# Kernel tuning notes

Hardware: AMD Instinct MI355X
Metric: run time of the kernel (lower is better)

Reference implementation:

```python
import jax, jax.numpy as jnp
import numpy as np

IN_CH, OUT_CH, K, UP = 512, 256, 3, 2
WSCALE = float(1.0 / np.sqrt(K * K * IN_CH))  # use_wscale gain / sqrt(fan_in), lr_mul=1
ACT_GAIN = float(np.sqrt(2.0))                # lrelu def_gain
CLAMP = 256.0                                  # conv_clamp * runtime_gain(=1)
FIR_PAD = 1                                    # px0+pxt = px1+pxt = 1 (derived in forward)

def _fir_filter():
    # upfirdn2d.setup_filter([1,3,3,1]): outer product then normalize to sum 1
    f1 = jnp.array([1.0, 3.0, 3.0, 1.0], jnp.float32)
    f2 = jnp.outer(f1, f1)
    return f2 / jnp.sum(f2)  # (4,4), sums to 1

def setup_inputs() -> dict:
    key = jax.random.key(0)
    k1, k2 = jax.random.split(key)
    return {
        "x": jax.random.normal(k1, (16, IN_CH, 64, 64), jnp.float32),
        "weight": jax.random.normal(k2, (OUT_CH, IN_CH, K, K), jnp.float32),
        "bias": jnp.zeros((OUT_CH,), jnp.float32),
    }

def _forward(x, weight, bias):
    w = weight * WSCALE  # runtime weight scaling
    # torch conv_transpose2d(x, w.transpose(0,1), stride=UP, padding=0)
    # == lhs-dilated correlation with spatially flipped kernel, pad K-1 each side
    k = w[:, :, ::-1, ::-1]
    y = jax.lax.conv_general_dilated(
        x, k, window_strides=(1, 1),
        padding=((K - 1, K - 1), (K - 1, K - 1)),
        lhs_dilation=(UP, UP),
        dimension_numbers=('NCHW', 'OIHW', 'NCHW'))  # (N, OUT_CH, 129, 129)
    # upfirdn2d(up=1, padding=(1,1,1,1), gain=UP**2):
    # pad, then depthwise conv with flipped filter scaled by gain**(ndim/2)=UP*UP
    f = _fir_filter() * (UP * UP)
    y = jnp.pad(y, ((0, 0), (0, 0), (FIR_PAD, FIR_PAD), (FIR_PAD, FIR_PAD)))
    fk = jnp.broadcast_to(f[::-1, ::-1][None, None], (OUT_CH, 1, 4, 4))
    y = jax.lax.conv_general_dilated(
        y, fk, (1, 1), 'VALID',
        feature_group_count=OUT_CH,
        dimension_numbers=('NCHW', 'OIHW', 'NCHW'))  # (N, OUT_CH, 128, 128)
    # bias_act: bias add, leaky_relu(0.2), gain sqrt(2), clamp +-256
    y = y + bias[None, :, None, None]
    y = jnp.where(y >= 0, y, 0.2 * y) * ACT_GAIN
    return jnp.clip(y, -CLAMP, CLAMP)

def reference(x, weight, bias):
    return _forward(x, weight, bias)
```

## Files before the change

kernel.cpp:

```cpp
#include <hip/hip_runtime.h>
#include <hip/hip_bf16.h>

#define NIMG 16
#define IN_CH 512
#define OUT_CH 256
#define HIN 64
#define HOUT 128
#define HP 66

#define WSCALE 0.014731391f
#define ACT_GAIN 1.41421356237f
#define CLAMP_V 256.0f

typedef __attribute__((ext_vector_type(8))) short bf16x8;
typedef __attribute__((ext_vector_type(4))) float f32x4;
typedef __attribute__((ext_vector_type(16))) float f32x16;

__device__ __constant__ float c_G[2][3][3] = {
    {{0.00f, 0.25f, 0.75f}, {0.75f, 0.75f, 0.25f}, {0.25f, 0.00f, 0.00f}},
    {{0.00f, 0.00f, 0.25f}, {0.25f, 0.75f, 0.75f}, {0.75f, 0.25f, 0.00f}}
};

#define XBF_BYTES ((size_t)NIMG * 64 * HP * HP * 16)
#define EBF_BYTES ((size_t)9 * 64 * 1024 * 16)
#define WS_NEED (XBF_BYTES + EBF_BYTES)

__global__ __launch_bounds__(256) void xpose_kernel(const float* __restrict__ x,
                                                    __hip_bfloat16* __restrict__ xbf) {
    const int n = blockIdx.z;
    const int hp = blockIdx.y;
    const int c0 = blockIdx.x << 6;
    const int tid = threadIdx.x;
    const int sgb = c0 >> 3;
    const bf16x8 zero = {0, 0, 0, 0, 0, 0, 0, 0};

    if (hp == 0 || hp == HP - 1) {
        for (int idx = tid; idx < 8 * HP; idx += 256) {
            int s3 = idx / HP, wp = idx - s3 * HP;
            size_t a = (((size_t)(n * 64 + sgb + s3) * HP + hp) * HP + wp);
            *(bf16x8*)((char*)xbf + a * 16) = zero;
        }
        return;
    }
    __shared__ float tile[64][65];
    {
        int cc = tid >> 6, w = tid & 63;
        for (int cb = 0; cb < 64; cb += 4)
            tile[cb + cc][w] =
                x[(((size_t)n * IN_CH + c0 + cb + cc) * HIN + (hp - 1)) * HIN + w];
    }
    __syncthreads();
    {
        int s3 = tid >> 5, wq = tid & 31;
#pragma unroll
        for (int wb = 0; wb < 64; wb += 32) {
            int wimg = wb + wq;
            bf16x8 v;
#pragma unroll
            for (int k = 0; k < 8; ++k) {
                __hip_bfloat16 b = __float2bfloat16(tile[s3 * 8 + k][wimg]);
                v[k] = *reinterpret_cast<short*>(&b);
            }
            size_t a = (((size_t)(n * 64 + sgb + s3) * HP + hp) * HP + (wimg + 1));
            *(bf16x8*)((char*)xbf + a * 16) = v;
        }
        if (tid < 16) {
            int s3h = tid >> 1, wph = (tid & 1) ? (HP - 1) : 0;
            size_t a = (((size_t)(n * 64 + sgb + s3h) * HP + hp) * HP + wph);
            *(bf16x8*)((char*)xbf + a * 16) = zero;
        }
    }
}

__global__ __launch_bounds__(256) void build_ebf_kernel(const float* __restrict__ w,
                                                        __hip_bfloat16* __restrict__ ebf) {
    int gid = blockIdx.x * 256 + threadIdx.x;
    if (gid >= OUT_CH * IN_CH) return;
    int oc = gid >> 9, c = gid & 511;
    int sg = c >> 3, ce = c & 7;
    float wm[3][3];
    const float* wp = w + (size_t)gid * 9;
#pragma unroll
    for (int a = 0; a < 3; ++a)
#pragma unroll
        for (int b = 0; b < 3; ++b) wm[a][b] = wp[a * 3 + b] * WSCALE;
#pragma unroll
    for (int i = 0; i < 3; ++i)
#pragma unroll
        for (int j = 0; j < 3; ++j)
#pragma unroll
            for (int pu = 0; pu < 2; ++pu)
#pragma unroll
                for (int pv = 0; pv < 2; ++pv) {
                    float s = 0.f;
#pragma unroll
                    for (int a = 0; a < 3; ++a)
#pragma unroll
                        for (int b = 0; b < 3; ++b)
                            s += wm[a][b] * c_G[pu][i][a] * c_G[pv][j][b];
                    int row = oc * 4 + pu * 2 + pv;
                    ebf[(((size_t)(i * 3 + j) * 64 + sg) * 1024 + row) * 8 + ce] =
                        __float2bfloat16(s);
                }
}

#define MFMA4(AF, BF)                                                                       \
    do {                                                                                    \
        acc[0] = __builtin_amdgcn_mfma_f32_32x32x16_bf16((AF)[0], (BF)[0], acc[0], 0, 0, 0);\
        acc[1] = __builtin_amdgcn_mfma_f32_32x32x16_bf16((AF)[0], (BF)[1], acc[1], 0, 0, 0);\
        acc[2] = __builtin_amdgcn_mfma_f32_32x32x16_bf16((AF)[1], (BF)[0], acc[2], 0, 0, 0);\
        acc[3] = __builtin_amdgcn_mfma_f32_32x32x16_bf16((AF)[1], (BF)[1], acc[3], 0, 0, 0);\
    } while (0)

#define ASTEP 557568
#define AJ_FJ (-3902960)
#define AJ_FI (-3901952)
#define BSTEP 131072
#define DAK1(PAR) (((((PAR) ^ 1) << 2) | 1) << 14)
#define DBK1(PAR) (((((PAR) ^ 1) << 2) | 3) << 14)
#define DAK0(PAR) ((((PAR) << 2) | 0) << 14)
#define DBK0(PAR) ((((PAR) << 2) | 2) << 14)

#define GLL(SRC, DSTOFF)                                                          \
    __builtin_amdgcn_global_load_lds(                                             \
        (const __attribute__((address_space(1))) unsigned int*)(SRC),             \
        (__attribute__((address_space(3))) unsigned int*)(ldsW + (DSTOFF)), 16, 0, 0)

#define TILE_ITER(PAR, TT, SP01, SP23, VMS, LGK3, LAST)                           \
    {                                                                             \
        const int PB = (PAR) ? 65536 : 0;                                         \
                     \
        aO[0] = *(const bf16x8*)&lds[A0 + PB + 8192];                             \
        aO[1] = *(const bf16x8*)&lds[A1 + PB + 8192];                             \
        bO[0] = *(const bf16x8*)&lds[B0 + PB + 8192];                             \
        bO[1] = *(const bf16x8*)&lds[B1 + PB + 8192];                             \
        if (SP01) GLL(xbc + sA1 + voffA, DAK1(PAR));                              \
        sA1 += (((TT) & 7) == 6) ? (((TT) == 22 || (TT) == 46) ? AJ_FI : AJ_FJ)   \
                                 : ASTEP;                                         \
        asm volatile("s_waitcnt lgkmcnt(4)" ::: "memory");                        \
        __builtin_amdgcn_sched_barrier(0);                                        \
        __builtin_amdgcn_s_setprio(1);                                            \
        MFMA4(aE, bE);                                                            \
        __builtin_amdgcn_s_setprio(0);                                            \
        asm volatile("s_waitcnt " VMS ::: "memory");                              \
        __builtin_amdgcn_s_barrier();                                             \
        __builtin_amdgcn_sched_barrier(0);                                        \
                     \
        aE[0] = *(const bf16x8*)&lds[A0 + PB + 16384];                            \
        aE[1] = *(const bf16x8*)&lds[A1 + PB + 16384];                            \
        bE[0] = *(const bf16x8*)&lds[B0 + PB + 16384];                            \
        bE[1] = *(const bf16x8*)&lds[B1 + PB + 16384];                            \
        if (SP01) GLL(ebc + sB1 + voffB, DBK1(PAR));                              \
        sB1 += BSTEP;                                                             \
        asm volatile("s_waitcnt lgkmcnt(4)" ::: "memory");                        \
        __builtin_amdgcn_sched_barrier(0);                                        \
        __builtin_amdgcn_s_setprio(1);                                            \
        MFMA4(aO, bO);                                                            \
        __builtin_amdgcn_s_setprio(0);                                            \
        __builtin_amdgcn_s_barrier();                                             \
        __builtin_amdgcn_sched_barrier(0);                                        \
                     \
        aO[0] = *(const bf16x8*)&lds[A0 + PB + 24576];                            \
        aO[1] = *(const bf16x8*)&lds[A1 + PB + 24576];                            \
        bO[0] = *(const bf16x8*)&lds[B0 + PB + 24576];                            \
        bO[1] = *(const bf16x8*)&lds[B1 + PB + 24576];                            \
        if (SP23) GLL(xbc + sA0 + voffA, DAK0(PAR));                              \
        sA0 += (((TT) & 7) == 5) ? (((TT) == 21 || (TT) == 45) ? AJ_FI : AJ_FJ)   \
                                 : ASTEP;                                         \
        asm volatile("s_waitcnt lgkmcnt(4)" ::: "memory");                        \
        __builtin_amdgcn_sched_barrier(0);                                        \
        __builtin_amdgcn_s_setprio(1);                                            \
        MFMA4(aE, bE);                                                            \
        __builtin_amdgcn_s_setprio(0);                                            \
        asm volatile("s_waitcnt " VMS ::: "memory");                              \
        __builtin_amdgcn_s_barrier();                                             \
        __builtin_amdgcn_sched_barrier(0);                                        \
           \
        if (!(LAST)) {                                                            \
            const int NB = (PAR) ? 0 : 65536;                                     \
            aE[0] = *(const bf16x8*)&lds[A0 + NB];                                \
            aE[1] = *(const bf16x8*)&lds[A1 + NB];                                \
            bE[0] = *(const bf16x8*)&lds[B0 + NB];                                \
            bE[1] = *(const bf16x8*)&lds[B1 + NB];                                \
        }                                                                         \
        if (SP23) GLL(ebc + sB0 + voffB, DBK0(PAR));                              \
        sB0 += BSTEP;                                                             \
        asm volatile("s_waitcnt " LGK3 ::: "memory");                             \
        __builtin_amdgcn_sched_barrier(0);                                        \
        __builtin_amdgcn_s_setprio(1);                                            \
        MFMA4(aO, bO);                                                            \
        __builtin_amdgcn_s_setprio(0);                                            \
        __builtin_amdgcn_s_barrier();                                             \
        __builtin_amdgcn_sched_barrier(0);                                        \
    }

__global__ __launch_bounds__(1024) void mfma_conv8_kernel(
    const __hip_bfloat16* __restrict__ xbf, const __hip_bfloat16* __restrict__ ebf,
    const float* __restrict__ bias, float* __restrict__ out) {
    __shared__ __align__(16) char lds[131072];

    const int tid = threadIdx.x;
    const int lane = tid & 63;
    const int wid = tid >> 6;
    const int wy = wid >> 2;
    const int wx = wid & 3;

    const int bid = blockIdx.x;
    const int wkid = ((bid & 7) << 7) + (bid >> 3);
    const int mtile = wkid >> 2;
    const int ntile = wkid & 3;
    const int n = mtile >> 4;
    const int sub = mtile & 15;
    const int qh0 = (sub >> 2) << 4;
    const int qw0 = (sub & 3) << 4;
    const int n0 = ntile << 8;

    const int slice = wid & 3;
    const int rb = wid >> 2;

    f32x16 acc[4];
#pragma unroll
    for (int j = 0; j < 4; ++j) acc[j] = (f32x16)(0.f);

    char* ldsW = lds + (slice << 12) + (rb << 10);
    const char* xbc = (const char*)xbf;
    const char* ebc = (const char*)ebf;

    const int q = lane ^ ((lane & 32) ? 4 : 0) ^ ((slice & 1) ? 4 : 0);
    const int voffA =
        ((((n << 6) + slice) * HP + qh0 + (rb << 2) + (q >> 4)) * HP + qw0 +
         (q & 15)) * 16;
    const int voffB = (slice << 14) + ((n0 + (rb << 6) + q) << 4);

    auto stage = [&](int s) {
        const int tt2 = s >> 2;
        const int part = s & 3;
        const int mat = part & 1;
        const int kh = part >> 1;
        const int slot = (((tt2 & 1) << 2) | (mat << 1) | kh) << 14;
        const int sg = (tt2 << 3) + (kh << 2);
        const char* src = mat == 0 ? (xbc + voffA + sg * 69696)
                                   : (ebc + voffB + sg * 16384);
        GLL(src, slot);
    };

    const int sl = lane >> 5;
    const int l31 = lane & 31;
    const int sx = sl ? 64 : 0;
    const int A0 = (sl << 12) + (wy << 10) + ((l31 << 4) ^ sx);
    const int A1 = (sl << 12) + (wy << 10) + 512 + ((l31 << 4) ^ 64 ^ sx);
    const int B0 = 32768 + (sl << 12) + (wx << 10) + ((l31 << 4) ^ sx);
    const int B1 = 32768 + (sl << 12) + (wx << 10) + 512 + ((l31 << 4) ^ 64 ^ sx);

    int sA1 = 12 * 69696;
    int sA0 = 16 * 69696;
    int sB1 = 12 * 16384;
    int sB0 = 16 * 16384;

#pragma unroll
    for (int s = 0; s < 6; ++s) stage(s);
    asm volatile("s_waitcnt vmcnt(2)" ::: "memory");
    __builtin_amdgcn_s_barrier();
    __builtin_amdgcn_sched_barrier(0);

    bf16x8 aE[2], aO[2], bE[2], bO[2];
    aE[0] = *(const bf16x8*)&lds[A0];
    aE[1] = *(const bf16x8*)&lds[A1];
    bE[0] = *(const bf16x8*)&lds[B0];
    bE[1] = *(const bf16x8*)&lds[B1];

#pragma unroll 1
    for (int tt = 0; tt < 68; tt += 2) {
        TILE_ITER(0, tt, 1, 1, "vmcnt(3)", "lgkmcnt(4)", 0);
        TILE_ITER(1, tt + 1, 1, 1, "vmcnt(3)", "lgkmcnt(4)", 0);
    }
    TILE_ITER(0, 68, 1, 1, "vmcnt(3)", "lgkmcnt(4)", 0);
    TILE_ITER(1, 69, 1, 1, "vmcnt(0)", "lgkmcnt(4)", 0);
    TILE_ITER(0, 70, 1, 0, "vmcnt(0)", "lgkmcnt(4)", 0);
    TILE_ITER(1, 71, 0, 0, "vmcnt(0)", "lgkmcnt(0)", 1);

    float bv[2];
#pragma unroll
    for (int nt = 0; nt < 2; ++nt)
        bv[nt] = bias[(n0 + (wx << 6) + (nt << 5) + l31) >> 2];
#pragma unroll
    for (int j = 0; j < 4; ++j) {
        const int mt = j >> 1, nt = j & 1;
        const int nn = n0 + (wx << 6) + (nt << 5) + l31;
        const int oc = nn >> 2, pu = (nn >> 1) & 1, pv = nn & 1;
#pragma unroll
        for (int v = 0; v < 16; ++v) {
            const int m = (wy << 6) + (mt << 5) + (v & 3) + ((v >> 2) << 3) + (sl << 2);
            const int qr = m >> 4, qc = m & 15;
            const int hb = 2 * (qh0 + qr), wb = 2 * (qw0 + qc);
            float val = acc[j][v] + bv[nt];
            val = (val >= 0.f ? val : 0.2f * val) * ACT_GAIN;
            val = fminf(fmaxf(val, -CLAMP_V), CLAMP_V);
            out[(((size_t)n * OUT_CH + oc) * HOUT + (hb + pu)) * HOUT + (wb + pv)] = val;
        }
    }
}

__global__ void build_e_kernel(const float* __restrict__ w, float* __restrict__ e_ws) {
    int gid = blockIdx.x * blockDim.x + threadIdx.x;
    if (gid >= OUT_CH * IN_CH) return;
    float wm[3][3];
    const float* wp = w + (size_t)gid * 9;
#pragma unroll
    for (int a = 0; a < 3; ++a)
#pragma unroll
        for (int b = 0; b < 3; ++b) wm[a][b] = wp[a * 3 + b] * WSCALE;
    float* op = e_ws + (size_t)gid * 36;
#pragma unroll
    for (int i = 0; i < 3; ++i)
#pragma unroll
        for (int j = 0; j < 3; ++j)
#pragma unroll
            for (int pu = 0; pu < 2; ++pu)
#pragma unroll
                for (int pv = 0; pv < 2; ++pv) {
                    float s = 0.f;
#pragma unroll
                    for (int a = 0; a < 3; ++a)
#pragma unroll
                        for (int b = 0; b < 3; ++b)
                            s += wm[a][b] * c_G[pu][i][a] * c_G[pv][j][b];
                    op[(i * 3 + j) * 4 + pu * 2 + pv] = s;
                }
}

#define OGB 8
#define CB 8
#define QT 16
__global__ __launch_bounds__(256) void fused_conv_kernel(
    const float* __restrict__ x, const float* __restrict__ e_ws,
    const float* __restrict__ bias, float* __restrict__ out) {
    __shared__ float sX[CB][18][19];
    __shared__ float4 sE[OGB * CB * 9];
    const int tid = threadIdx.x;
    const int o2 = tid >> 7;
    const int qy = (tid >> 3) & 15;
    const int qxp = tid & 7;
    const int tileIdx = blockIdx.x;
    const int hq0 = (tileIdx >> 2) * QT;
    const int wq0 = (tileIdx & 3) * QT;
    const int o0 = blockIdx.y * OGB;
    const int n = blockIdx.z;
    float4 acc[2][4];
#pragma unroll
    for (int q = 0; q < 2; ++q)
#pragma unroll
        for (int oo = 0; oo < 4; ++oo) acc[q][oo] = make_float4(0.f, 0.f, 0.f, 0.f);
    for (int c0 = 0; c0 < IN_CH; c0 += CB) {
        for (int idx = tid; idx < CB * 18 * 18; idx += 256) {
            int cc = idx / 324;
            int rem = idx - cc * 324;
            int r = rem / 18;
            int col = rem - r * 18;
            int h = hq0 - 1 + r;
            int ww = wq0 - 1 + col;
            float v = 0.f;
            if (h >= 0 && h < HIN && ww >= 0 && ww < HIN)
                v = x[(((size_t)n * IN_CH + (c0 + cc)) * HIN + h) * HIN + ww];
            sX[cc][r][col] = v;
        }
        {
            float* sEf = (float*)sE;
            for (int idx = tid; idx < OGB * CB * 36; idx += 256) {
                int ol = idx / (CB * 36);
                int rem = idx - ol * (CB * 36);
                sEf[ol * (CB * 36) + rem] =
                    e_ws[((size_t)(o0 + ol) * IN_CH + c0) * 36 + rem];
            }
        }
        __syncthreads();
#pragma unroll 1
        for (int cc = 0; cc < CB; ++cc) {
#pragma unroll
            for (int i = 0; i < 3; ++i) {
#pragma unroll
                for (int j = 0; j < 3; ++j) {
                    float xv0 = sX[cc][qy + i][2 * qxp + j];
                    float xv1 = sX[cc][qy + i][2 * qxp + 1 + j];
#pragma unroll
                    for (int oo = 0; oo < 4; ++oo) {
                        float4 e = sE[((o2 * 4 + oo) * CB + cc) * 9 + i * 3 + j];
                        acc[0][oo].x += xv0 * e.x; acc[0][oo].y += xv0 * e.y;
                        acc[0][oo].z += xv0 * e.z; acc[0][oo].w += xv0 * e.w;
                        acc[1][oo].x += xv1 * e.x; acc[1][oo].y += xv1 * e.y;
                        acc[1][oo].z += xv1 * e.z; acc[1][oo].w += xv1 * e.w;
                    }
                }
            }
        }
        __syncthreads();
    }
#pragma unroll
    for (int q = 0; q < 2; ++q) {
        int qx = 2 * qxp + q;
        int u0 = 2 * (hq0 + qy);
        int v0 = 2 * (wq0 + qx);
#pragma unroll
        for (int oo = 0; oo < 4; ++oo) {
            int o = o0 + o2 * 4 + oo;
            float b = bias[o];
            float vals[4] = {acc[q][oo].x, acc[q][oo].y, acc[q][oo].z, acc[q][oo].w};
#pragma unroll
            for (int p = 0; p < 4; ++p) {
                int pu = p >> 1, pv = p & 1;
                float v = vals[p] + b;
                v = (v >= 0.f ? v : 0.2f * v) * ACT_GAIN;
                v = fminf(fmaxf(v, -CLAMP_V), CLAMP_V);
                out[(((size_t)n * OUT_CH + o) * HOUT + (u0 + pu)) * HOUT + (v0 + pv)] = v;
            }
        }
    }
}

extern "C" void kernel_launch(void* const* d_in, const int* in_sizes, int n_in,
                              void* d_out, int out_size, void* d_ws, size_t ws_size,
                              hipStream_t stream) {
    const float* x = (const float*)d_in[0];
    const float* w = (const float*)d_in[1];
    const float* bias = (const float*)d_in[2];
    float* out = (float*)d_out;

    if (ws_size >= WS_NEED) {
        __hip_bfloat16* xbf = (__hip_bfloat16*)d_ws;
        __hip_bfloat16* ebf = (__hip_bfloat16*)((char*)d_ws + XBF_BYTES);
        xpose_kernel<<<dim3(8, HP, NIMG), 256, 0, stream>>>(x, xbf);
        build_ebf_kernel<<<(OUT_CH * IN_CH + 255) / 256, 256, 0, stream>>>(w, ebf);
        mfma_conv8_kernel<<<dim3(1024), 1024, 0, stream>>>(xbf, ebf, bias, out);
    } else {
        float* e_ws = (float*)d_ws;
        build_e_kernel<<<(OUT_CH * IN_CH + 255) / 256, 256, 0, stream>>>(w, e_ws);
        dim3 grid(16, OUT_CH / OGB, NIMG);
        fused_conv_kernel<<<grid, 256, 0, stream>>>(x, e_ws, bias, out);
    }
}
```

Before: 651.3 us.

## Replace fine-grained staggered LDS prefetch with simple whole-tile double buffering

Replaces the staggered per-quarter prefetch pipeline, which issued one global-to-LDS load per sub-step and placed a barrier after every MFMA group, with a simpler scheme. Each tile now issues all four loads for the next buffer at its start, runs four MFMA groups, then waits on vmcnt(0) and does one barrier per tile. This cuts barrier count and simplifies waitcnt bookkeeping. In exchange the prefetch distance shrinks to one tile and every tile ends with a full memory drain, so load latency may be exposed.

```diff
diff --git a/kernel.cpp b/kernel.cpp
--- a/kernel.cpp
+++ b/kernel.cpp
@@ -116,82 +116,73 @@
 #define AJ_FJ (-3902960)
 #define AJ_FI (-3901952)
 #define BSTEP 131072
-#define DAK1(PAR) (((((PAR) ^ 1) << 2) | 1) << 14)
-#define DBK1(PAR) (((((PAR) ^ 1) << 2) | 3) << 14)
-#define DAK0(PAR) ((((PAR) << 2) | 0) << 14)
-#define DBK0(PAR) ((((PAR) << 2) | 2) << 14)
 
 #define GLL(SRC, DSTOFF)                                                          \
     __builtin_amdgcn_global_load_lds(                                             \
         (const __attribute__((address_space(1))) unsigned int*)(SRC),             \
         (__attribute__((address_space(3))) unsigned int*)(ldsW + (DSTOFF)), 16, 0, 0)
 
-#define TILE_ITER(PAR, TT, SP01, SP23, VMS, LGK3, LAST)                           \
+#define TILE_ITER(PAR, TT, SP, LAST)                                              \
     {                                                                             \
-        const int PB = (PAR) ? 65536 : 0;                                         \
-                     \
+        const int PB = (PAR) << 16;                                               \
+        const int NPB = ((PAR) ^ 1) << 16;                                        \
+            \
+        if (SP) {                                                                 \
+            GLL(xbc + sA0 + voffA, NPB);                                          \
+            GLL(xbc + sA1 + voffA, NPB + 16384);                                  \
+            GLL(ebc + sB0 + voffB, NPB + 32768);                                  \
+            GLL(ebc + sB1 + voffB, NPB + 49152);                                  \
+        }                                                                         \
+        sA0 += (((TT) & 7) == 6) ? (((TT) == 22 || (TT) == 46) ? AJ_FI : AJ_FJ)   \
+                                 : ASTEP;                                         \
+        sA1 += (((TT) & 7) == 6) ? (((TT) == 22 || (TT) == 46) ? AJ_FI : AJ_FJ)   \
+                                 : ASTEP;                                         \
+        sB0 += BSTEP;                                                             \
+        sB1 += BSTEP;                                                             \
+                                                  \
+        aE[0] = *(const bf16x8*)&lds[A0 + PB];                                    \
+        aE[1] = *(const bf16x8*)&lds[A1 + PB];                                    \
+        bE[0] = *(const bf16x8*)&lds[B0 + PB];                                    \
+        bE[1] = *(const bf16x8*)&lds[B1 + PB];                                    \
         aO[0] = *(const bf16x8*)&lds[A0 + PB + 8192];                             \
         aO[1] = *(const bf16x8*)&lds[A1 + PB + 8192];                             \
         bO[0] = *(const bf16x8*)&lds[B0 + PB + 8192];                             \
         bO[1] = *(const bf16x8*)&lds[B1 + PB + 8192];                             \
-        if (SP01) GLL(xbc + sA1 + voffA, DAK1(PAR));                              \
-        sA1 += (((TT) & 7) == 6) ? (((TT) == 22 || (TT) == 46) ? AJ_FI : AJ_FJ)   \
-                                 : ASTEP;                                         \
         asm volatile("s_waitcnt lgkmcnt(4)" ::: "memory");                        \
         __builtin_amdgcn_sched_barrier(0);                                        \
         __builtin_amdgcn_s_setprio(1);                                            \
         MFMA4(aE, bE);                                                            \
         __builtin_amdgcn_s_setprio(0);                                            \
-        asm volatile("s_waitcnt " VMS ::: "memory");                              \
-        __builtin_amdgcn_s_barrier();                                             \
-        __builtin_amdgcn_sched_barrier(0);                                        \
-                     \
+                                                                \
         aE[0] = *(const bf16x8*)&lds[A0 + PB + 16384];                            \
         aE[1] = *(const bf16x8*)&lds[A1 + PB + 16384];                            \
         bE[0] = *(const bf16x8*)&lds[B0 + PB + 16384];                            \
         bE[1] = *(const bf16x8*)&lds[B1 + PB + 16384];                            \
-        if (SP01) GLL(ebc + sB1 + voffB, DBK1(PAR));                              \
-        sB1 += BSTEP;                                                             \
         asm volatile("s_waitcnt lgkmcnt(4)" ::: "memory");                        \
         __builtin_amdgcn_sched_barrier(0);                                        \
         __builtin_amdgcn_s_setprio(1);                                            \
         MFMA4(aO, bO);                                                            \
         __builtin_amdgcn_s_setprio(0);                                            \
-        __builtin_amdgcn_s_barrier();                                             \
-        __builtin_amdgcn_sched_barrier(0);                                        \
-                     \
+                                                                \
         aO[0] = *(const bf16x8*)&lds[A0 + PB + 24576];                            \
         aO[1] = *(const bf16x8*)&lds[A1 + PB + 24576];                            \
         bO[0] = *(const bf16x8*)&lds[B0 + PB + 24576];                            \
         bO[1] = *(const bf16x8*)&lds[B1 + PB + 24576];                            \
-        if (SP23) GLL(xbc + sA0 + voffA, DAK0(PAR));                              \
-        sA0 += (((TT) & 7) == 5) ? (((TT) == 21 || (TT) == 45) ? AJ_FI : AJ_FJ)   \
-                                 : ASTEP;                                         \
         asm volatile("s_waitcnt lgkmcnt(4)" ::: "memory");                        \
         __builtin_amdgcn_sched_barrier(0);                                        \
         __builtin_amdgcn_s_setprio(1);                                            \
         MFMA4(aE, bE);                                                            \
         __builtin_amdgcn_s_setprio(0);                                            \
-        asm volatile("s_waitcnt " VMS ::: "memory");                              \
-        __builtin_amdgcn_s_barrier();                                             \
-        __builtin_amdgcn_sched_barrier(0);                                        \
-           \
-        if (!(LAST)) {                                                            \
-            const int NB = (PAR) ? 0 : 65536;                                     \
-            aE[0] = *(const bf16x8*)&lds[A0 + NB];                                \
-            aE[1] = *(const bf16x8*)&lds[A1 + NB];                                \
-            bE[0] = *(const bf16x8*)&lds[B0 + NB];                                \
-            bE[1] = *(const bf16x8*)&lds[B1 + NB];                                \
-        }                                                                         \
-        if (SP23) GLL(ebc + sB0 + voffB, DBK0(PAR));                              \
-        sB0 += BSTEP;                                                             \
-        asm volatile("s_waitcnt " LGK3 ::: "memory");                             \
+        asm volatile("s_waitcnt lgkmcnt(0)" ::: "memory");                        \
         __builtin_amdgcn_sched_barrier(0);                                        \
         __builtin_amdgcn_s_setprio(1);                                            \
         MFMA4(aO, bO);                                                            \
         __builtin_amdgcn_s_setprio(0);                                            \
-        __builtin_amdgcn_s_barrier();                                             \
-        __builtin_amdgcn_sched_barrier(0);                                        \
+        if (!(LAST)) {                                                            \
+            asm volatile("s_waitcnt vmcnt(0)" ::: "memory");                      \
+            __builtin_amdgcn_s_barrier();                                         \
+            __builtin_amdgcn_sched_barrier(0);                                    \
+        }                                                                         \
     }
 
 __global__ __launch_bounds__(1024) void mfma_conv8_kernel(
@@ -232,18 +223,6 @@
          (q & 15)) * 16;
     const int voffB = (slice << 14) + ((n0 + (rb << 6) + q) << 4);
 
-    auto stage = [&](int s) {
-        const int tt2 = s >> 2;
-        const int part = s & 3;
-        const int mat = part & 1;
-        const int kh = part >> 1;
-        const int slot = (((tt2 & 1) << 2) | (mat << 1) | kh) << 14;
-        const int sg = (tt2 << 3) + (kh << 2);
-        const char* src = mat == 0 ? (xbc + voffA + sg * 69696)
-                                   : (ebc + voffB + sg * 16384);
-        GLL(src, slot);
-    };
-
     const int sl = lane >> 5;
     const int l31 = lane & 31;
     const int sx = sl ? 64 : 0;
@@ -252,32 +231,28 @@
     const int B0 = 32768 + (sl << 12) + (wx << 10) + ((l31 << 4) ^ sx);
     const int B1 = 32768 + (sl << 12) + (wx << 10) + 512 + ((l31 << 4) ^ 64 ^ sx);
 
+    int sA0 = 8 * 69696;
     int sA1 = 12 * 69696;
-    int sA0 = 16 * 69696;
+    int sB0 = 8 * 16384;
     int sB1 = 12 * 16384;
-    int sB0 = 16 * 16384;
-
-#pragma unroll
-    for (int s = 0; s < 6; ++s) stage(s);
-    asm volatile("s_waitcnt vmcnt(2)" ::: "memory");
+
+    GLL(xbc + voffA, 0);
+    GLL(xbc + voffA + 4 * 69696, 16384);
+    GLL(ebc + voffB, 32768);
+    GLL(ebc + voffB + 4 * 16384, 49152);
+    asm volatile("s_waitcnt vmcnt(0)" ::: "memory");
     __builtin_amdgcn_s_barrier();
     __builtin_amdgcn_sched_barrier(0);
 
     bf16x8 aE[2], aO[2], bE[2], bO[2];
-    aE[0] = *(const bf16x8*)&lds[A0];
-    aE[1] = *(const bf16x8*)&lds[A1];
-    bE[0] = *(const bf16x8*)&lds[B0];
-    bE[1] = *(const bf16x8*)&lds[B1];
 
 #pragma unroll 1
-    for (int tt = 0; tt < 68; tt += 2) {
-        TILE_ITER(0, tt, 1, 1, "vmcnt(3)", "lgkmcnt(4)", 0);
-        TILE_ITER(1, tt + 1, 1, 1, "vmcnt(3)", "lgkmcnt(4)", 0);
-    }
-    TILE_ITER(0, 68, 1, 1, "vmcnt(3)", "lgkmcnt(4)", 0);
-    TILE_ITER(1, 69, 1, 1, "vmcnt(0)", "lgkmcnt(4)", 0);
-    TILE_ITER(0, 70, 1, 0, "vmcnt(0)", "lgkmcnt(4)", 0);
-    TILE_ITER(1, 71, 0, 0, "vmcnt(0)", "lgkmcnt(0)", 1);
+    for (int tt = 0; tt < 70; tt += 2) {
+        TILE_ITER(0, tt, 1, 0);
+        TILE_ITER(1, tt + 1, 1, 0);
+    }
+    TILE_ITER(0, 70, 1, 0);
+    TILE_ITER(1, 71, 0, 1);
 
     float bv[2];
 #pragma unroll
```

Result: slower. 679.0 us (+4.2%).
